# Optimization experiments

Measured on AMD Instinct MI355X. Metric: run time of the kernel, lower is better.

The kernel has to match this reference:

```python
import jax, jax.numpy as jnp
import numpy as np

MIN_NORM = 1e-15
BALL_EPS = 1e-3   # project() margin from ball boundary (c = 1)
TANH_CLIP = 15.0


def _norm(x):
    return jnp.sqrt(jnp.sum(x * x, axis=-1, keepdims=True)).clip(MIN_NORM)


def _tanh(x):
    return jnp.tanh(jnp.clip(x, -TANH_CLIP, TANH_CLIP))


def _artanh(x):
    return jnp.arctanh(jnp.clip(x, -1.0 + 1e-7, 1.0 - 1e-7))


def mobius_add(x, y):
    # Poincare ball Mobius addition, curvature c = 1
    x2 = jnp.sum(x * x, axis=-1, keepdims=True)
    y2 = jnp.sum(y * y, axis=-1, keepdims=True)
    xy = jnp.sum(x * y, axis=-1, keepdims=True)
    num = (1.0 + 2.0 * xy + y2) * x + (1.0 - x2) * y
    den = 1.0 + 2.0 * xy + x2 * y2
    return num / den.clip(MIN_NORM)


def project(x):
    norm = _norm(x)
    maxnorm = 1.0 - BALL_EPS
    return jnp.where(norm > maxnorm, x * (maxnorm / norm), x)


def expmap0(u):
    # exp map at the origin
    n = _norm(u)
    return _tanh(n) * u / n


def expmap(u, p):
    # exp map of tangent vector u at base point p
    n = _norm(u)
    p2 = jnp.sum(p * p, axis=-1, keepdims=True)
    lam = 2.0 / (1.0 - p2).clip(MIN_NORM)
    second = _tanh(0.5 * lam * n) * u / n
    return mobius_add(p, second)


def logmap(y, x):
    # log map of point y at base point x
    sub = mobius_add(-x, y)
    n = _norm(sub)
    x2 = jnp.sum(x * x, axis=-1, keepdims=True)
    lam = 2.0 / (1.0 - x2).clip(MIN_NORM)
    return (2.0 / lam) * _artanh(n) * sub / n


def setup_inputs() -> dict:
    key = jax.random.key(0)
    k1, k2, k3, k4 = jax.random.split(key, 4)
    n_entities, n_edges, n_rel, d = 100000, 800000, 32, 64
    # scale embeddings down so points stay well inside the unit ball
    ego_embed = 0.1 * jax.random.normal(k1, (n_entities, d), dtype=jnp.float32)
    relation_embed = 0.1 * jax.random.normal(k2, (n_rel, d), dtype=jnp.float32)
    edge_index = jax.random.randint(k3, (2, n_edges), 0, n_entities, dtype=jnp.int64)
    edge_type = jax.random.randint(k4, (n_edges,), 0, n_rel, dtype=jnp.int64)
    return {"ego_embed": ego_embed, "edge_index": edge_index,
            "edge_type": edge_type, "relation_embed": relation_embed}


def reference(ego_embed, edge_index, edge_type, relation_embed):
    head, tail = edge_index[0], edge_index[1]
    n_entities = ego_embed.shape[0]
    head_emb = ego_embed[head]          # [E, d] gather
    tail_emb = ego_embed[tail]          # [E, d] gather
    relation_emb = relation_embed[edge_type]  # [E, d] gather
    hyper_head = expmap0(head_emb)
    hyper_tail = expmap(tail_emb, hyper_head)
    hyper_rel = expmap(relation_emb, hyper_head)
    res = project(mobius_add(hyper_tail, hyper_rel))
    res = logmap(res, hyper_head)
    # scatter_mean over head index
    sums = jax.ops.segment_sum(res, head, num_segments=n_entities)
    counts = jax.ops.segment_sum(jnp.ones((head.shape[0],), dtype=res.dtype),
                                 head, num_segments=n_entities)
    entity_agg = sums / jnp.maximum(counts, 1.0)[:, None]
    return entity_agg
```

## Files before the change

kernel.cpp:

```cpp
#include <hip/hip_runtime.h>
#include <math.h>

#define D 64
#define MAXNORM 0.999f
#define MAXNORM2 (0.999f * 0.999f)
#define MIN_NORM 1e-15f
#define TANH_CLIP 15.0f
#define CHUNK 1024

struct f4 { float x, y, z, w; };

__device__ __forceinline__ float frcp(float x) { return __builtin_amdgcn_rcpf(x); }
__device__ __forceinline__ float frsq(float x) { return __builtin_amdgcn_rsqf(x); }

__device__ __forceinline__ float dot8p(const f4& a0, const f4& a1,
                                       const f4& b0, const f4& b1) {
    return a0.x * b0.x + a0.y * b0.y + a0.z * b0.z + a0.w * b0.w +
           a1.x * b1.x + a1.y * b1.y + a1.z * b1.z + a1.w * b1.w;
}

__device__ __forceinline__ float rsum8(float v) {
    v += __shfl_xor(v, 1);
    v += __shfl_xor(v, 2);
    v += __shfl_xor(v, 4);
    return v;
}


__global__ void hist_kernel(const int* __restrict__ eidx,
                            int* __restrict__ cnt,
                            int* __restrict__ rank, int E) {
    int e = blockIdx.x * blockDim.x + threadIdx.x;
    if (e < E) rank[e] = atomicAdd(&cnt[eidx[e]], 1);
}


__global__ void scan_kernel(const int* __restrict__ cnt,
                            int* __restrict__ off,
                            const float* __restrict__ ego,
                            const float* __restrict__ rel,
                            float* __restrict__ norms,
                            float* __restrict__ relnorm,
                            float2* __restrict__ scal,
                            int N, int NB, int E) {
    if (blockIdx.x >= NB) {
        int wid = (blockIdx.x - NB) * 4 + (threadIdx.x >> 6);
        int lane = threadIdx.x & 63;
        if (wid >= N + 32) return;
        const float* src = (wid < N) ? (ego + (size_t)wid * D)
                                     : (rel + (size_t)(wid - N) * D);
        float v = src[lane];
        float s = v * v;
        s += __shfl_xor(s, 1);  s += __shfl_xor(s, 2);  s += __shfl_xor(s, 4);
        s += __shfl_xor(s, 8);  s += __shfl_xor(s, 16); s += __shfl_xor(s, 32);
        if (lane == 0) {
            float nh = sqrtf(s);
            if (wid < N) {
                norms[wid] = nh;
                float nhc = fmaxf(nh, MIN_NORM);
                float eh  = __expf(-2.0f * fminf(nhc, TANH_CLIP));
                float fp  = (1.0f - eh) * frcp((1.0f + eh) * nhc);
                float th2 = fp * fp * nhc * nhc;
                float tol = fmaxf(1.0f - th2, MIN_NORM);
                scal[wid] = make_float2(fp, tol);
            } else {
                relnorm[wid - N] = nh;
            }
        }
        return;
    }

    __shared__ int sdata[256];
    __shared__ int sprefix;
    int tid = threadIdx.x;
    int base0 = blockIdx.x * CHUNK;

    if (blockIdx.x == 0 && tid == 0) off[N] = E;

    int psum = 0;
    const int4* cnt4 = (const int4*)cnt;
    for (int i = tid; i < (base0 >> 2); i += 256) {
        int4 v = cnt4[i];
        psum += v.x + v.y + v.z + v.w;
    }
    sdata[tid] = psum;
    __syncthreads();
    for (int o = 128; o > 0; o >>= 1) {
        if (tid < o) sdata[tid] += sdata[tid + o];
        __syncthreads();
    }
    if (tid == 0) sprefix = sdata[0];
    __syncthreads();
    int prefix = sprefix;
    __syncthreads();

    int base = base0 + tid * 4;
    int v0 = (base + 0 < N) ? cnt[base + 0] : 0;
    int v1 = (base + 1 < N) ? cnt[base + 1] : 0;
    int v2 = (base + 2 < N) ? cnt[base + 2] : 0;
    int v3 = (base + 3 < N) ? cnt[base + 3] : 0;
    sdata[tid] = v0 + v1 + v2 + v3;
    __syncthreads();
    for (int o = 1; o < 256; o <<= 1) {
        int add = (tid >= o) ? sdata[tid - o] : 0;
        __syncthreads();
        sdata[tid] += add;
        __syncthreads();
    }
    int run = prefix + ((tid > 0) ? sdata[tid - 1] : 0);
    if (base + 0 < N) { off[base + 0] = run; run += v0; }
    if (base + 1 < N) { off[base + 1] = run; run += v1; }
    if (base + 2 < N) { off[base + 2] = run; run += v2; }
    if (base + 3 < N) { off[base + 3] = run; run += v3; }
}

__global__ void scatter_kernel(const int* __restrict__ eidx,
                               const int* __restrict__ etype,
                               const int* __restrict__ rank,
                               const int* __restrict__ off,
                               int* __restrict__ sorted, int E) {
    int e = blockIdx.x * blockDim.x + threadIdx.x;
    if (e < E) {
        int pos = off[eidx[e]] + rank[e];
        sorted[pos] = eidx[E + e] | (etype[e] << 17);
    }
}


__global__ void __launch_bounds__(256) agg_kernel(
        const float* __restrict__ ego,
        const float* __restrict__ rel,
        const int* __restrict__ off,
        const int* __restrict__ sorted,
        const float* __restrict__ norms,
        const float* __restrict__ relnorm,
        const float2* __restrict__ scal,
        float* __restrict__ out,
        int N) {
    int wid = (blockIdx.x * blockDim.x + threadIdx.x) >> 6;
    if (wid >= N) return;
    int lane = threadIdx.x & 63;
    int slot = lane >> 3;
    int sub  = lane & 7;

    int h = wid;
    const float* hrow = ego + (size_t)h * D;
    f4 h0 = *(const f4*)(hrow + sub * 4);
    f4 h1 = *(const f4*)(hrow + 32 + sub * 4);

    float2 sc2 = scal[h];
    float fp  = sc2.x;
    float tol = sc2.y;
    float p2  = 1.0f - tol;
    float hl  = frcp(tol);

    int o = off[h];
    int c = off[h + 1] - o;
    f4 a0 = {0.f, 0.f, 0.f, 0.f}, a1 = {0.f, 0.f, 0.f, 0.f};
    float accP = 0.f;

    for (int i = slot; i < c; i += 8) {
        int pk   = sorted[o + i];
        int tail = pk & 0x1FFFF;
        int type = pk >> 17;

        const float* trow = ego + (size_t)tail * D;
        f4 t0 = *(const f4*)(trow + sub * 4);
        f4 t1 = *(const f4*)(trow + 32 + sub * 4);
        const float* rrow = rel + (size_t)type * D;
        f4 r0 = *(const f4*)(rrow + sub * 4);
        f4 r1 = *(const f4*)(rrow + 32 + sub * 4);
        float nt = norms[tail];
        float nr = relnorm[type];

        float d_ht = rsum8(dot8p(h0, h1, t0, t1));
        float d_hr = rsum8(dot8p(h0, h1, r0, r1));
        float d_tr = rsum8(dot8p(t0, t1, r0, r1));

        float t2 = nt * nt, r2 = nr * nr;
        float pt = fp * d_ht;
        float pr = fp * d_hr;

        float ntc = fmaxf(nt, MIN_NORM);
        float et  = __expf(-2.0f * fminf(hl * ntc, TANH_CLIP));
        float ft  = (1.0f - et) * frcp((1.0f + et) * ntc);
        float pyt = ft * pt;
        float yt2 = ft * ft * t2;
        float o1t = fmaf(2.0f, pyt, 1.0f);
        float at  = o1t + yt2;
        float invt = frcp(fmaxf(fmaf(p2, yt2, o1t), MIN_NORM));
        float At = at * invt;
        float Bt = tol * invt * ft;
        float x2 = (at - tol) * invt;

        float nrc = fmaxf(nr, MIN_NORM);
        float er  = __expf(-2.0f * fminf(hl * nrc, TANH_CLIP));
        float fr  = (1.0f - er) * frcp((1.0f + er) * nrc);
        float pyr = fr * pr;
        float yr2 = fr * fr * r2;
        float o1r = fmaf(2.0f, pyr, 1.0f);
        float ar  = o1r + yr2;
        float invr = frcp(fmaxf(fmaf(p2, yr2, o1r), MIN_NORM));
        float Ar = ar * invr;
        float Br = tol * invr * fr;
        float y2 = (ar - tol) * invr;

        float xy = At * Ar * p2 + At * Br * pr + Ar * Bt * pt + Bt * Br * d_tr;
        float o1m = fmaf(2.0f, xy, 1.0f);
        float am = o1m + y2;
        float bm = 1.0f - x2;
        float invm = frcp(fmaxf(fmaf(x2, y2, o1m), MIN_NORM));
        float al = (am * At + bm * Ar) * invm;
        float be = am * Bt * invm;
        float ga = bm * Br * invm;
        float m2 = fmaxf((am - bm) * invm, 1e-30f);

        if (m2 > MAXNORM2) {
            float s_ = MAXNORM * frsq(m2);
            al *= s_; be *= s_; ga *= s_;
            m2 = MAXNORM2;
        }

        float pm   = al * p2 + be * pt + ga * pr;
        float o2   = fmaf(-2.0f, pm, 1.0f);
        float invs = frcp(fmaxf(fmaf(p2, m2, o2), MIN_NORM));
        float om   = o2 + m2;
        float smm  = tol * invs;
        float u = fmaf(smm, al, -om * invs);
        float v = smm * be;
        float w = smm * ga;
        float s2 = fmaxf((om - tol) * invs, 1e-30f);

        float irs = frsq(s2);
        float ns  = fminf(s2 * irs, 1.0f - 1e-7f);
        float art = 0.5f * __logf((1.0f + ns) * frcp(1.0f - ns));
        float scv = tol * art * irs;

        float ct = scv * v, cr = scv * w;
        accP = fmaf(scv, u, accP);
        a0.x += ct * t0.x + cr * r0.x;  a0.y += ct * t0.y + cr * r0.y;
        a0.z += ct * t0.z + cr * r0.z;  a0.w += ct * t0.w + cr * r0.w;
        a1.x += ct * t1.x + cr * r1.x;  a1.y += ct * t1.y + cr * r1.y;
        a1.z += ct * t1.z + cr * r1.z;  a1.w += ct * t1.w + cr * r1.w;
    }

    #define RED(x) x += __shfl_xor(x, 8); x += __shfl_xor(x, 16); x += __shfl_xor(x, 32);
    RED(accP)
    RED(a0.x) RED(a0.y) RED(a0.z) RED(a0.w)
    RED(a1.x) RED(a1.y) RED(a1.z) RED(a1.w)
    #undef RED

    if (slot == 0) {
        float invc = frcp(fmaxf((float)c, 1.0f));
        float hp = accP * fp * invc;
        f4 o0, o1;
        o0.x = hp * h0.x + a0.x * invc;  o0.y = hp * h0.y + a0.y * invc;
        o0.z = hp * h0.z + a0.z * invc;  o0.w = hp * h0.w + a0.w * invc;
        o1.x = hp * h1.x + a1.x * invc;  o1.y = hp * h1.y + a1.y * invc;
        o1.z = hp * h1.z + a1.z * invc;  o1.w = hp * h1.w + a1.w * invc;
        float* orow = out + (size_t)h * D;
        *(f4*)(orow + sub * 4)      = o0;
        *(f4*)(orow + 32 + sub * 4) = o1;
    }
}

extern "C" void kernel_launch(void* const* d_in, const int* in_sizes, int n_in,
                              void* d_out, int out_size, void* d_ws, size_t ws_size,
                              hipStream_t stream) {
    const float* ego  = (const float*)d_in[0];
    const int*   eidx = (const int*)d_in[1];
    const int*   etyp = (const int*)d_in[2];
    const float* rel  = (const float*)d_in[3];
    float* out = (float*)d_out;

    int E = in_sizes[1] / 2;
    int N = in_sizes[0] / D;
    int NB = (N + CHUNK - 1) / CHUNK;

    float2* scal  = (float2*)d_ws;
    int* cnt      = (int*)(scal + N);
    int* off      = cnt + N;
    int* rank     = off + N + 1;
    int* sorted   = rank + E;
    float* norms   = (float*)(sorted + E);
    float* relnorm = norms + N;

    hipMemsetAsync(cnt, 0, (size_t)N * sizeof(int), stream);

    const int tpb = 256;
    int hist_blocks = (E + tpb - 1) / tpb;
    int norm_blocks = (N + 32 + 3) / 4;

    hist_kernel<<<hist_blocks, tpb, 0, stream>>>(eidx, cnt, rank, E);
    scan_kernel<<<NB + norm_blocks, tpb, 0, stream>>>(cnt, off, ego, rel,
                                                      norms, relnorm, scal,
                                                      N, NB, E);
    scatter_kernel<<<hist_blocks, tpb, 0, stream>>>(eidx, etyp, rank, off, sorted, E);

    int nblocks = (N + 3) / 4;
    agg_kernel<<<nblocks, tpb, 0, stream>>>(ego, rel, off, sorted,
                                            norms, relnorm, scal, out, N);
}
```

Before: 166.4 us.

## Split per-edge scalar chain into thread-per-edge kernel feeding coefficient-based accumulation

```diff
diff --git a/kernel.cpp b/kernel.cpp
--- a/kernel.cpp
+++ b/kernel.cpp
@@ -12,19 +12,6 @@
 
 __device__ __forceinline__ float frcp(float x) { return __builtin_amdgcn_rcpf(x); }
 __device__ __forceinline__ float frsq(float x) { return __builtin_amdgcn_rsqf(x); }
-
-__device__ __forceinline__ float dot8p(const f4& a0, const f4& a1,
-                                       const f4& b0, const f4& b1) {
-    return a0.x * b0.x + a0.y * b0.y + a0.z * b0.z + a0.w * b0.w +
-           a1.x * b1.x + a1.y * b1.y + a1.z * b1.z + a1.w * b1.w;
-}
-
-__device__ __forceinline__ float rsum8(float v) {
-    v += __shfl_xor(v, 1);
-    v += __shfl_xor(v, 2);
-    v += __shfl_xor(v, 4);
-    return v;
-}
 
 
 __global__ void hist_kernel(const int* __restrict__ eidx,
@@ -127,13 +114,123 @@
 }
 
 
-__global__ void __launch_bounds__(256) agg_kernel(
+__global__ void __launch_bounds__(256) chain_kernel(
+        const float* __restrict__ ego,
+        const float* __restrict__ rel,
+        const int* __restrict__ eidx,
+        const int* __restrict__ etyp,
+        const int* __restrict__ rank,
+        const int* __restrict__ off,
+        const float* __restrict__ norms,
+        const float* __restrict__ relnorm,
+        const float2* __restrict__ scal,
+        float4* __restrict__ coeff,
+        int E) {
+    int e = blockIdx.x * blockDim.x + threadIdx.x;
+    if (e >= E) return;
+
+    int head = eidx[e];
+    int tail = eidx[E + e];
+    int type = etyp[e];
+
+    const float* hrow = ego + (size_t)head * D;
+    const float* trow = ego + (size_t)tail * D;
+    const float* rrow = rel + (size_t)type * D;
+
+    f4 aht = {0.f,0.f,0.f,0.f}, ahr = {0.f,0.f,0.f,0.f}, atr = {0.f,0.f,0.f,0.f};
+    #pragma unroll
+    for (int k = 0; k < 16; k++) {
+        f4 hh = *(const f4*)(hrow + k * 4);
+        f4 tt = *(const f4*)(trow + k * 4);
+        f4 rr = *(const f4*)(rrow + k * 4);
+        aht.x += hh.x * tt.x; aht.y += hh.y * tt.y;
+        aht.z += hh.z * tt.z; aht.w += hh.w * tt.w;
+        ahr.x += hh.x * rr.x; ahr.y += hh.y * rr.y;
+        ahr.z += hh.z * rr.z; ahr.w += hh.w * rr.w;
+        atr.x += tt.x * rr.x; atr.y += tt.y * rr.y;
+        atr.z += tt.z * rr.z; atr.w += tt.w * rr.w;
+    }
+    float d_ht = (aht.x + aht.y) + (aht.z + aht.w);
+    float d_hr = (ahr.x + ahr.y) + (ahr.z + ahr.w);
+    float d_tr = (atr.x + atr.y) + (atr.z + atr.w);
+
+    float2 sc2 = scal[head];
+    float fp  = sc2.x;
+    float tol = sc2.y;
+    float p2  = 1.0f - tol;
+    float hl  = frcp(tol);
+    float nt  = norms[tail];
+    float nr  = relnorm[type];
+
+    float t2 = nt * nt, r2 = nr * nr;
+    float pt = fp * d_ht;
+    float pr = fp * d_hr;
+
+    float ntc = fmaxf(nt, MIN_NORM);
+    float et  = __expf(-2.0f * fminf(hl * ntc, TANH_CLIP));
+    float ft  = (1.0f - et) * frcp((1.0f + et) * ntc);
+    float pyt = ft * pt;
+    float yt2 = ft * ft * t2;
+    float o1t = fmaf(2.0f, pyt, 1.0f);
+    float at  = o1t + yt2;
+    float invt = frcp(fmaxf(fmaf(p2, yt2, o1t), MIN_NORM));
+    float At = at * invt;
+    float Bt = tol * invt * ft;
+    float x2 = (at - tol) * invt;
+
+    float nrc = fmaxf(nr, MIN_NORM);
+    float er  = __expf(-2.0f * fminf(hl * nrc, TANH_CLIP));
+    float fr  = (1.0f - er) * frcp((1.0f + er) * nrc);
+    float pyr = fr * pr;
+    float yr2 = fr * fr * r2;
+    float o1r = fmaf(2.0f, pyr, 1.0f);
+    float ar  = o1r + yr2;
+    float invr = frcp(fmaxf(fmaf(p2, yr2, o1r), MIN_NORM));
+    float Ar = ar * invr;
+    float Br = tol * invr * fr;
+    float y2 = (ar - tol) * invr;
+
+    float xy = At * Ar * p2 + At * Br * pr + Ar * Bt * pt + Bt * Br * d_tr;
+    float o1m = fmaf(2.0f, xy, 1.0f);
+    float am = o1m + y2;
+    float bm = 1.0f - x2;
+    float invm = frcp(fmaxf(fmaf(x2, y2, o1m), MIN_NORM));
+    float al = (am * At + bm * Ar) * invm;
+    float be = am * Bt * invm;
+    float ga = bm * Br * invm;
+    float m2 = fmaxf((am - bm) * invm, 1e-30f);
+
+    if (m2 > MAXNORM2) {
+        float s_ = MAXNORM * frsq(m2);
+        al *= s_; be *= s_; ga *= s_;
+        m2 = MAXNORM2;
+    }
+
+    float pm   = al * p2 + be * pt + ga * pr;
+    float o2   = fmaf(-2.0f, pm, 1.0f);
+    float invs = frcp(fmaxf(fmaf(p2, m2, o2), MIN_NORM));
+    float om   = o2 + m2;
+    float smm  = tol * invs;
+    float u = fmaf(smm, al, -om * invs);
+    float v = smm * be;
+    float w = smm * ga;
+    float s2 = fmaxf((om - tol) * invs, 1e-30f);
+
+    float irs = frsq(s2);
+    float ns  = fminf(s2 * irs, 1.0f - 1e-7f);
+    float art = 0.5f * __logf((1.0f + ns) * frcp(1.0f - ns));
+    float scv = tol * art * irs;
+
+    coeff[off[head] + rank[e]] = make_float4(scv * u, scv * v, scv * w, 0.f);
+}
+
+
+__global__ void __launch_bounds__(256) accum_kernel(
         const float* __restrict__ ego,
         const float* __restrict__ rel,
         const int* __restrict__ off,
         const int* __restrict__ sorted,
-        const float* __restrict__ norms,
-        const float* __restrict__ relnorm,
+        const float4* __restrict__ coeff,
         const float2* __restrict__ scal,
         float* __restrict__ out,
         int N) {
@@ -144,23 +241,14 @@
     int sub  = lane & 7;
 
     int h = wid;
-    const float* hrow = ego + (size_t)h * D;
-    f4 h0 = *(const f4*)(hrow + sub * 4);
-    f4 h1 = *(const f4*)(hrow + 32 + sub * 4);
-
-    float2 sc2 = scal[h];
-    float fp  = sc2.x;
-    float tol = sc2.y;
-    float p2  = 1.0f - tol;
-    float hl  = frcp(tol);
-
     int o = off[h];
     int c = off[h + 1] - o;
     f4 a0 = {0.f, 0.f, 0.f, 0.f}, a1 = {0.f, 0.f, 0.f, 0.f};
     float accP = 0.f;
 
     for (int i = slot; i < c; i += 8) {
-        int pk   = sorted[o + i];
+        int pk     = sorted[o + i];
+        float4 cf  = coeff[o + i];
         int tail = pk & 0x1FFFF;
         int type = pk >> 17;
 
@@ -170,74 +258,9 @@
         const float* rrow = rel + (size_t)type * D;
         f4 r0 = *(const f4*)(rrow + sub * 4);
         f4 r1 = *(const f4*)(rrow + 32 + sub * 4);
-        float nt = norms[tail];
-        float nr = relnorm[type];
-
-        float d_ht = rsum8(dot8p(h0, h1, t0, t1));
-        float d_hr = rsum8(dot8p(h0, h1, r0, r1));
-        float d_tr = rsum8(dot8p(t0, t1, r0, r1));
-
-        float t2 = nt * nt, r2 = nr * nr;
-        float pt = fp * d_ht;
-        float pr = fp * d_hr;
-
-        float ntc = fmaxf(nt, MIN_NORM);
-        float et  = __expf(-2.0f * fminf(hl * ntc, TANH_CLIP));
-        float ft  = (1.0f - et) * frcp((1.0f + et) * ntc);
-        float pyt = ft * pt;
-        float yt2 = ft * ft * t2;
-        float o1t = fmaf(2.0f, pyt, 1.0f);
-        float at  = o1t + yt2;
-        float invt = frcp(fmaxf(fmaf(p2, yt2, o1t), MIN_NORM));
-        float At = at * invt;
-        float Bt = tol * invt * ft;
-        float x2 = (at - tol) * invt;
-
-        float nrc = fmaxf(nr, MIN_NORM);
-        float er  = __expf(-2.0f * fminf(hl * nrc, TANH_CLIP));
-        float fr  = (1.0f - er) * frcp((1.0f + er) * nrc);
-        float pyr = fr * pr;
-        float yr2 = fr * fr * r2;
-        float o1r = fmaf(2.0f, pyr, 1.0f);
-        float ar  = o1r + yr2;
-        float invr = frcp(fmaxf(fmaf(p2, yr2, o1r), MIN_NORM));
-        float Ar = ar * invr;
-        float Br = tol * invr * fr;
-        float y2 = (ar - tol) * invr;
-
-        float xy = At * Ar * p2 + At * Br * pr + Ar * Bt * pt + Bt * Br * d_tr;
-        float o1m = fmaf(2.0f, xy, 1.0f);
-        float am = o1m + y2;
-        float bm = 1.0f - x2;
-        float invm = frcp(fmaxf(fmaf(x2, y2, o1m), MIN_NORM));
-        float al = (am * At + bm * Ar) * invm;
-        float be = am * Bt * invm;
-        float ga = bm * Br * invm;
-        float m2 = fmaxf((am - bm) * invm, 1e-30f);
-
-        if (m2 > MAXNORM2) {
-            float s_ = MAXNORM * frsq(m2);
-            al *= s_; be *= s_; ga *= s_;
-            m2 = MAXNORM2;
-        }
-
-        float pm   = al * p2 + be * pt + ga * pr;
-        float o2   = fmaf(-2.0f, pm, 1.0f);
-        float invs = frcp(fmaxf(fmaf(p2, m2, o2), MIN_NORM));
-        float om   = o2 + m2;
-        float smm  = tol * invs;
-        float u = fmaf(smm, al, -om * invs);
-        float v = smm * be;
-        float w = smm * ga;
-        float s2 = fmaxf((om - tol) * invs, 1e-30f);
-
-        float irs = frsq(s2);
-        float ns  = fminf(s2 * irs, 1.0f - 1e-7f);
-        float art = 0.5f * __logf((1.0f + ns) * frcp(1.0f - ns));
-        float scv = tol * art * irs;
-
-        float ct = scv * v, cr = scv * w;
-        accP = fmaf(scv, u, accP);
+
+        float ct = cf.y, cr = cf.z;
+        accP += cf.x;
         a0.x += ct * t0.x + cr * r0.x;  a0.y += ct * t0.y + cr * r0.y;
         a0.z += ct * t0.z + cr * r0.z;  a0.w += ct * t0.w + cr * r0.w;
         a1.x += ct * t1.x + cr * r1.x;  a1.y += ct * t1.y + cr * r1.y;
@@ -251,6 +274,10 @@
     #undef RED
 
     if (slot == 0) {
+        const float* hrow = ego + (size_t)h * D;
+        f4 h0 = *(const f4*)(hrow + sub * 4);
+        f4 h1 = *(const f4*)(hrow + 32 + sub * 4);
+        float fp = scal[h].x;
         float invc = frcp(fmaxf((float)c, 1.0f));
         float hp = accP * fp * invc;
         f4 o0, o1;
@@ -277,7 +304,8 @@
     int N = in_sizes[0] / D;
     int NB = (N + CHUNK - 1) / CHUNK;
 
-    float2* scal  = (float2*)d_ws;
+    float4* coeff = (float4*)d_ws;
+    float2* scal  = (float2*)(coeff + E);
     int* cnt      = (int*)(scal + N);
     int* off      = cnt + N;
     int* rank     = off + N + 1;
@@ -288,16 +316,18 @@
     hipMemsetAsync(cnt, 0, (size_t)N * sizeof(int), stream);
 
     const int tpb = 256;
-    int hist_blocks = (E + tpb - 1) / tpb;
+    int eblocks = (E + tpb - 1) / tpb;
     int norm_blocks = (N + 32 + 3) / 4;
 
-    hist_kernel<<<hist_blocks, tpb, 0, stream>>>(eidx, cnt, rank, E);
+    hist_kernel<<<eblocks, tpb, 0, stream>>>(eidx, cnt, rank, E);
     scan_kernel<<<NB + norm_blocks, tpb, 0, stream>>>(cnt, off, ego, rel,
                                                       norms, relnorm, scal,
                                                       N, NB, E);
-    scatter_kernel<<<hist_blocks, tpb, 0, stream>>>(eidx, etyp, rank, off, sorted, E);
+    scatter_kernel<<<eblocks, tpb, 0, stream>>>(eidx, etyp, rank, off, sorted, E);
+    chain_kernel<<<eblocks, tpb, 0, stream>>>(ego, rel, eidx, etyp, rank, off,
+                                              norms, relnorm, scal, coeff, E);
 
     int nblocks = (N + 3) / 4;
-    agg_kernel<<<nblocks, tpb, 0, stream>>>(ego, rel, off, sorted,
-                                            norms, relnorm, scal, out, N);
-}
+    accum_kernel<<<nblocks, tpb, 0, stream>>>(ego, rel, off, sorted, coeff,
+                                              scal, out, N);
+}
```

Measured after the change: 284.7 us. +71.1%, slower.

## Precompute per-edge tail scalars in scatter and pack into sorted payload

Applied to the files above, without the earlier changes.

```diff
diff --git a/kernel.cpp b/kernel.cpp
--- a/kernel.cpp
+++ b/kernel.cpp
@@ -114,16 +114,33 @@
     if (base + 3 < N) { off[base + 3] = run; run += v3; }
 }
 
+
 __global__ void scatter_kernel(const int* __restrict__ eidx,
                                const int* __restrict__ etype,
                                const int* __restrict__ rank,
                                const int* __restrict__ off,
-                               int* __restrict__ sorted, int E) {
+                               const float* __restrict__ norms,
+                               const float2* __restrict__ scal,
+                               float4* __restrict__ payA, int E) {
     int e = blockIdx.x * blockDim.x + threadIdx.x;
-    if (e < E) {
-        int pos = off[eidx[e]] + rank[e];
-        sorted[pos] = eidx[E + e] | (etype[e] << 17);
-    }
+    if (e >= E) return;
+    int head = eidx[e];
+    int tail = eidx[E + e];
+    int type = etype[e];
+    int pos  = off[head] + rank[e];
+
+    float2 sc2 = scal[head];
+    float fp  = sc2.x;
+    float tol = sc2.y;
+    float hl  = frcp(tol);
+    float nt  = norms[tail];
+    float ntc = fmaxf(nt, MIN_NORM);
+    float et  = __expf(-2.0f * fminf(hl * ntc, TANH_CLIP));
+    float ft  = (1.0f - et) * frcp((1.0f + et) * ntc);
+    float gt  = ft * nt;
+
+    payA[pos] = make_float4(__int_as_float(tail | (type << 17)),
+                            fp * ft, gt * gt, tol * ft);
 }
 
 
@@ -131,8 +148,7 @@
         const float* __restrict__ ego,
         const float* __restrict__ rel,
         const int* __restrict__ off,
-        const int* __restrict__ sorted,
-        const float* __restrict__ norms,
+        const float4* __restrict__ payA,
         const float* __restrict__ relnorm,
         const float2* __restrict__ scal,
         float* __restrict__ out,
@@ -160,7 +176,8 @@
     float accP = 0.f;
 
     for (int i = slot; i < c; i += 8) {
-        int pk   = sorted[o + i];
+        float4 pa = payA[o + i];
+        int pk   = __float_as_int(pa.x);
         int tail = pk & 0x1FFFF;
         int type = pk >> 17;
 
@@ -170,46 +187,42 @@
         const float* rrow = rel + (size_t)type * D;
         f4 r0 = *(const f4*)(rrow + sub * 4);
         f4 r1 = *(const f4*)(rrow + 32 + sub * 4);
-        float nt = norms[tail];
         float nr = relnorm[type];
 
         float d_ht = rsum8(dot8p(h0, h1, t0, t1));
         float d_hr = rsum8(dot8p(h0, h1, r0, r1));
         float d_tr = rsum8(dot8p(t0, t1, r0, r1));
 
-        float t2 = nt * nt, r2 = nr * nr;
         float pt = fp * d_ht;
         float pr = fp * d_hr;
 
-        float ntc = fmaxf(nt, MIN_NORM);
-        float et  = __expf(-2.0f * fminf(hl * ntc, TANH_CLIP));
-        float ft  = (1.0f - et) * frcp((1.0f + et) * ntc);
-        float pyt = ft * pt;
-        float yt2 = ft * ft * t2;
+        float pyt = pa.y * d_ht;
+        float yt2 = pa.z;
         float o1t = fmaf(2.0f, pyt, 1.0f);
         float at  = o1t + yt2;
-        float invt = frcp(fmaxf(fmaf(p2, yt2, o1t), MIN_NORM));
+        float invt = frcp(fmaf(p2, yt2, o1t));
         float At = at * invt;
-        float Bt = tol * invt * ft;
+        float Bt = pa.w * invt;
         float x2 = (at - tol) * invt;
 
         float nrc = fmaxf(nr, MIN_NORM);
         float er  = __expf(-2.0f * fminf(hl * nrc, TANH_CLIP));
         float fr  = (1.0f - er) * frcp((1.0f + er) * nrc);
         float pyr = fr * pr;
-        float yr2 = fr * fr * r2;
+        float gr  = fr * nr;
+        float yr2 = gr * gr;
         float o1r = fmaf(2.0f, pyr, 1.0f);
         float ar  = o1r + yr2;
-        float invr = frcp(fmaxf(fmaf(p2, yr2, o1r), MIN_NORM));
+        float invr = frcp(fmaf(p2, yr2, o1r));
         float Ar = ar * invr;
-        float Br = tol * invr * fr;
+        float Br = tol * fr * invr;
         float y2 = (ar - tol) * invr;
 
         float xy = At * Ar * p2 + At * Br * pr + Ar * Bt * pt + Bt * Br * d_tr;
         float o1m = fmaf(2.0f, xy, 1.0f);
         float am = o1m + y2;
         float bm = 1.0f - x2;
-        float invm = frcp(fmaxf(fmaf(x2, y2, o1m), MIN_NORM));
+        float invm = frcp(fmaf(x2, y2, o1m));
         float al = (am * At + bm * Ar) * invm;
         float be = am * Bt * invm;
         float ga = bm * Br * invm;
@@ -223,7 +236,7 @@
 
         float pm   = al * p2 + be * pt + ga * pr;
         float o2   = fmaf(-2.0f, pm, 1.0f);
-        float invs = frcp(fmaxf(fmaf(p2, m2, o2), MIN_NORM));
+        float invs = frcp(fmaf(p2, m2, o2));
         float om   = o2 + m2;
         float smm  = tol * invs;
         float u = fmaf(smm, al, -om * invs);
@@ -277,27 +290,28 @@
     int N = in_sizes[0] / D;
     int NB = (N + CHUNK - 1) / CHUNK;
 
-    float2* scal  = (float2*)d_ws;
+    float4* payA  = (float4*)d_ws;
+    float2* scal  = (float2*)(payA + E);
     int* cnt      = (int*)(scal + N);
     int* off      = cnt + N;
     int* rank     = off + N + 1;
-    int* sorted   = rank + E;
-    float* norms   = (float*)(sorted + E);
+    float* norms   = (float*)(rank + E);
     float* relnorm = norms + N;
 
     hipMemsetAsync(cnt, 0, (size_t)N * sizeof(int), stream);
 
     const int tpb = 256;
-    int hist_blocks = (E + tpb - 1) / tpb;
+    int eblocks = (E + tpb - 1) / tpb;
     int norm_blocks = (N + 32 + 3) / 4;
 
-    hist_kernel<<<hist_blocks, tpb, 0, stream>>>(eidx, cnt, rank, E);
+    hist_kernel<<<eblocks, tpb, 0, stream>>>(eidx, cnt, rank, E);
     scan_kernel<<<NB + norm_blocks, tpb, 0, stream>>>(cnt, off, ego, rel,
                                                       norms, relnorm, scal,
                                                       N, NB, E);
-    scatter_kernel<<<hist_blocks, tpb, 0, stream>>>(eidx, etyp, rank, off, sorted, E);
+    scatter_kernel<<<eblocks, tpb, 0, stream>>>(eidx, etyp, rank, off,
+                                                norms, scal, payA, E);
 
     int nblocks = (N + 3) / 4;
-    agg_kernel<<<nblocks, tpb, 0, stream>>>(ego, rel, off, sorted,
-                                            norms, relnorm, scal, out, N);
-}
+    agg_kernel<<<nblocks, tpb, 0, stream>>>(ego, rel, off, payA,
+                                            relnorm, scal, out, N);
+}
```

Result: slower. 170.3 us (+2.3%).
